# Kernel tuning notes

Hardware: AMD Instinct MI355X
Metric: run time of the kernel (lower is better)

Reference implementation:

```python
import jax, jax.numpy as jnp
import numpy as np
from jax import lax

B, C, H, W = 256, 64, 48, 48   # batch, in_channels, spatial_dim, spatial_dim
E = 5                           # num_experts (ConditionalConv2D default)
DIM = 64 + 1                    # n_regulators + 1


def setup_inputs() -> dict:
    key = jax.random.key(0)
    ks = jax.random.split(key, 24)
    def n(k, shape, s=0.05):
        return jax.random.normal(k, shape, jnp.float32) * s
    inp = {
        "spatial_maps": jax.random.normal(ks[0], (B, C, H, W), jnp.float32),
        "cluster_info": jax.random.randint(ks[1], (B,), 0, C),
        # ConditionalConv2D (1x1, num_experts=5)
        "expert_w": n(ks[2], (E, C, C)),          # [experts, out_c, in_c] (1x1 squeezed)
        "cond_b": n(ks[3], (C,)),
        "route_emb": n(ks[4], (C, 4 * C)),        # Embedding(num_clusters=C, pool_emb=4C)
        "route_W": n(ks[5], (E, 8 * C)),          # Linear(2*pool_emb -> E)
        "route_b": n(ks[6], (E,)),
        # weight-normed conv stack (v, g, bias, prelu-a)
        "v1": n(ks[7], (32, C, 3, 3)),  "g1": jnp.ones((32,), jnp.float32),  "cb1": n(ks[8], (32,)),  "a1": jnp.array(0.1, jnp.float32),
        "v2": n(ks[9], (64, 32, 3, 3)), "g2": jnp.ones((64,), jnp.float32),  "cb2": n(ks[10], (64,)), "a2": jnp.array(0.1, jnp.float32),
        "v3": n(ks[11], (128, 64, 3, 3)), "g3": jnp.ones((128,), jnp.float32), "cb3": n(ks[12], (128,)), "a3": jnp.array(0.1, jnp.float32),
        # cluster embedding + alpha + MLP
        "emb2": n(ks[13], (C, 128)),
        "alpha": jnp.array(1.0, jnp.float32),
        "mW1": n(ks[14], (64, 128)), "mb1": n(ks[15], (64,)), "a4": jnp.array(0.1, jnp.float32),
        "mW2": n(ks[16], (32, 64)),  "mb2": n(ks[17], (32,)), "a5": jnp.array(0.1, jnp.float32),
        "mW3": n(ks[18], (DIM, 32)), "mb3": n(ks[19], (DIM,)),
    }
    return inp


def _wn(v, g):
    # weight_norm over all dims except 0 (torch default dim=0)
    nrm = jnp.sqrt((v * v).sum((1, 2, 3)))
    return v * (g / nrm)[:, None, None, None]


def _conv(x, w, b):
    y = lax.conv_general_dilated(x, w, (1, 1), 'SAME',
                                 dimension_numbers=('NCHW', 'OIHW', 'NCHW'))
    return y + b[None, :, None, None]


def _prelu(x, a):
    return jnp.where(x >= 0, x, a * x)


def _mpool(x):
    return lax.reduce_window(x, -jnp.inf, lax.max, (1, 1, 2, 2), (1, 1, 2, 2), 'VALID')


def reference(spatial_maps, cluster_info, expert_w, cond_b, route_emb, route_W, route_b,
              v1, g1, cb1, a1, v2, g2, cb2, a2, v3, g3, cb3, a3,
              emb2, alpha, mW1, mb1, a4, mW2, mb2, a5, mW3, mb3):
    x = spatial_maps
    # routing: adaptive avg pool (2,2), flatten, concat cluster embedding, linear, sigmoid
    pooled = x.reshape(B, C, 2, H // 2, 2, W // 2).mean((3, 5)).reshape(B, 4 * C)
    feat = jnp.concatenate([pooled, route_emb[cluster_info]], axis=1)      # [B, 8C]
    rw = jax.nn.sigmoid(feat @ route_W.T + route_b)                        # [B, E]
    # per-sample expert-mixed 1x1 kernel, applied as batched 1x1 conv
    kern = jnp.einsum('be,eoi->boi', rw, expert_w)                         # [B, C, C]
    cc = jnp.einsum('boi,bihw->bohw', kern, x) + cond_b[None, :, None, None]
    out = jax.nn.sigmoid(cc) * x                                           # attention gate
    # dense conv stack
    h = _mpool(_prelu(_conv(out, _wn(v1, g1), cb1), a1))
    h = _mpool(_prelu(_conv(h, _wn(v2, g2), cb2), a2))
    h = _mpool(_prelu(_conv(h, _wn(v3, g3), cb3), a3))
    h = h.mean((2, 3))                                                      # AdaptiveAvgPool2d(1)+Flatten -> [B,128]
    h = h + emb2[cluster_info] * alpha
    # MLP head
    h = _prelu(h @ mW1.T + mb1, a4)
    h = _prelu(h @ mW2.T + mb2, a5)
    return h @ mW3.T + mb3                                                  # [B, DIM]
```

## Files before the change

### kernel.cpp

```cpp
#include <hip/hip_runtime.h>


typedef _Float16 f16;
typedef f16 f16x8 __attribute__((ext_vector_type(8)));
typedef f16 f16x4 __attribute__((ext_vector_type(4)));
typedef float f32x4 __attribute__((ext_vector_type(4)));

constexpr size_t OFF_POOLED = 0;
constexpr size_t OFF_KERN   = 65536;
constexpr size_t OFF_W1     = 65536 + 1048576;
constexpr size_t OFF_W2     = OFF_W1 + 32*64*12;
constexpr size_t OFF_W3     = OFF_W2 + 64*32*12;
constexpr size_t OFF_H1     = OFF_W3 + 128*64*12;

__device__ __forceinline__ float sigmoidf_(float z) {
    return 1.0f / (1.0f + __expf(-z));
}

__device__ __forceinline__ void store_slot8(f16* glds, int row, int sc, int icg, const float* c) {
    f16x8 hv = { (f16)c[0], (f16)c[1], (f16)c[2], (f16)c[3],
                 (f16)c[4], (f16)c[5], (f16)c[6], (f16)c[7] };
    *(f16x8*)&glds[(row * 50 + sc) * 64 + ((icg ^ (sc & 7)) << 3)] = hv;
}

__global__ void k_wnorm(const float* __restrict__ v1, const float* __restrict__ g1,
                        const float* __restrict__ v2, const float* __restrict__ g2,
                        const float* __restrict__ v3, const float* __restrict__ g3,
                        float* __restrict__ ws)
{
    int bo = blockIdx.x;
    const float* v; const float* g; int IC, oc; int which;
    if (bo < 32)       { v = v1; g = g1; oc = bo;      IC = 64; which = 1; }
    else if (bo < 96)  { v = v2; g = g2; oc = bo - 32; IC = 32; which = 2; }
    else               { v = v3; g = g3; oc = bo - 96; IC = 64; which = 3; }
    int n = IC * 9;
    const float* vo = v + (size_t)oc * n;
    float s = 0.0f;
    for (int i = threadIdx.x; i < n; i += 256) { float xv = vo[i]; s += xv * xv; }
    __shared__ float swarp[4];
    __shared__ float sscale;
    int lane = threadIdx.x & 63, wid = threadIdx.x >> 6;
    #pragma unroll
    for (int off = 32; off; off >>= 1) s += __shfl_down(s, off);
    if (lane == 0) swarp[wid] = s;
    __syncthreads();
    if (threadIdx.x == 0) {
        float tsum = swarp[0] + swarp[1] + swarp[2] + swarp[3];
        sscale = g[oc] / sqrtf(tsum);
    }
    __syncthreads();
    float sc = sscale;
    if (which == 1) {
        f16* o1 = (f16*)(ws + OFF_W1);
        for (int i = threadIdx.x; i < n; i += 256) {
            int ic = i / 9, kk = i - ic * 9;
            o1[kk * 2048 + oc * 64 + (ic ^ ((oc & 7) << 3))] = (f16)(vo[i] * sc);
        }
    } else if (which == 2) {
        f16* o2 = (f16*)(ws + OFF_W2);
        for (int i = threadIdx.x; i < n; i += 256) {
            int ic = i / 9, kk = i - ic * 9;
            o2[(kk * 64 + oc) * 32 + ic] = (f16)(vo[i] * sc);
        }
    } else {
        f16* o3 = (f16*)(ws + OFF_W3);
        for (int i = threadIdx.x; i < n; i += 256) {
            int ic = i / 9, kk = i - ic * 9;
            o3[(kk * 128 + oc) * 64 + ic] = (f16)(vo[i] * sc);
        }
    }
}

__global__ void __launch_bounds__(64)
k_pool(const float* __restrict__ x, float* __restrict__ ws)
{
    int bc = blockIdx.x;
    int lane = threadIdx.x;
    const float4* p = (const float4*)(x + (size_t)bc * 2304);
    float a0 = 0.f, a1 = 0.f, a2 = 0.f, a3 = 0.f;
    #pragma unroll
    for (int j = 0; j < 9; j++) {
        int i = lane + 64 * j;
        int row = i / 12, cg = i - 12 * row;
        float4 v = p[i];
        float s = v.x + v.y + v.z + v.w;
        bool hq = (row >= 24), wq = (cg >= 6);
        a0 += (!hq && !wq) ? s : 0.f;
        a1 += (!hq &&  wq) ? s : 0.f;
        a2 += ( hq && !wq) ? s : 0.f;
        a3 += ( hq &&  wq) ? s : 0.f;
    }
    #pragma unroll
    for (int off = 32; off; off >>= 1) {
        a0 += __shfl_down(a0, off);
        a1 += __shfl_down(a1, off);
        a2 += __shfl_down(a2, off);
        a3 += __shfl_down(a3, off);
    }
    if (lane == 0) {
        int b = bc >> 6, c = bc & 63;
        float* d = ws + OFF_POOLED + (size_t)b * 256 + c * 4;
        d[0] = a0 * (1.0f / 576.0f);
        d[1] = a1 * (1.0f / 576.0f);
        d[2] = a2 * (1.0f / 576.0f);
        d[3] = a3 * (1.0f / 576.0f);
    }
}

__global__ void k_route(const int* __restrict__ cluster,
                        const float* __restrict__ route_emb,
                        const float* __restrict__ route_W,
                        const float* __restrict__ route_b,
                        const float* __restrict__ expert_w,
                        float* __restrict__ ws)
{
    int b = blockIdx.x, t = threadIdx.x;
    __shared__ float feat[512];
    __shared__ float rwv[5];
    __shared__ float red[256];
    int cl = cluster[b];
    feat[t]       = ws[OFF_POOLED + (size_t)b * 256 + t];
    feat[256 + t] = route_emb[(size_t)cl * 256 + t];
    __syncthreads();
    float f0 = feat[t], f1 = feat[256 + t];
    for (int e = 0; e < 5; e++) {
        float pv = f0 * route_W[e * 512 + t] + f1 * route_W[e * 512 + 256 + t];
        red[t] = pv;
        __syncthreads();
        if (t < 128) red[t] += red[t + 128];
        __syncthreads();
        if (t < 64) {
            float s = red[t] + red[t + 64];
            #pragma unroll
            for (int off = 32; off; off >>= 1) s += __shfl_down(s, off);
            if (t == 0) rwv[e] = sigmoidf_(s + route_b[e]);
        }
        __syncthreads();
    }
    float r0 = rwv[0], r1 = rwv[1], r2 = rwv[2], r3 = rwv[3], r4 = rwv[4];
    f16* khg = (f16*)(ws + OFF_KERN);
    for (int j = t; j < 4096; j += 256) {
        int oc = j >> 6, ic = j & 63;
        float kv = r0 * expert_w[j] + r1 * expert_w[4096 + j] +
                   r2 * expert_w[2 * 4096 + j] + r3 * expert_w[3 * 4096 + j] +
                   r4 * expert_w[4 * 4096 + j];
        khg[(size_t)b * 4096 + oc * 64 + (ic ^ ((oc & 7) << 3))] = (f16)kv;
    }
}

__global__ void __launch_bounds__(512, 4)
k_f1(const float* __restrict__ x, const f16* __restrict__ kernH,
     const float* __restrict__ cond_b, const f16* __restrict__ w1H,
     const float* __restrict__ cb1, const float* __restrict__ a1,
     f16* __restrict__ h1h)
{
    extern __shared__ char smem[];
    f16*  glds  = (f16*)smem;
    f16*  kh    = (f16*)(smem + 64000);
    float* cbl  = (float*)(smem + 72192);
    float* dump = (float*)smem;
    f16*  poolt = (f16*)(smem + 52224);

    const int t = threadIdx.x;
    const int tile = blockIdx.x;
    const int b = blockIdx.y;
    const int r0 = tile * 8;
    const int w = t >> 6, l = t & 63;
    const int l15 = l & 15, agrp = l >> 4;

    ((uint4*)kh)[t] = ((const uint4*)(kernH + (size_t)b * 4096))[t];
    if (t < 64) cbl[t] = cond_b[t];
    if (t < 160) {
        int row = t >> 4, rem = t & 15;
        int col = (rem >= 8) ? 49 : 0;
        int slot = rem & 7;
        uint4 z = {};
        *(uint4*)&glds[(row * 50 + col) * 64 + slot * 8] = z;
    }
    for (int e = t; e < 960; e += 512) {
        int row = e / 96;
        int rem = e - row * 96;
        int colg = rem >> 3;
        int icg = rem & 7;
        int r_in = r0 - 1 + row;
        float4 va[8];
        if (r_in >= 0 && r_in < 48) {
            const float4* xp = (const float4*)x + ((size_t)(b * 64 + icg * 8)) * 576 + r_in * 12 + colg;
            #pragma unroll
            for (int i = 0; i < 8; i++) va[i] = xp[i * 576];
        } else {
            #pragma unroll
            for (int i = 0; i < 8; i++) va[i] = (float4){0.f, 0.f, 0.f, 0.f};
        }
        float c0[8], c1[8], c2c[8], c3[8];
        #pragma unroll
        for (int i = 0; i < 8; i++) { c0[i] = va[i].x; c1[i] = va[i].y; c2c[i] = va[i].z; c3[i] = va[i].w; }
        int scb = colg * 4 + 1;
        store_slot8(glds, row, scb + 0, icg, c0);
        store_slot8(glds, row, scb + 1, icg, c1);
        store_slot8(glds, row, scb + 2, icg, c2c);
        store_slot8(glds, row, scb + 3, icg, c3);
    }
    __syncthreads();

    {
        const int nt0 = (w < 6) ? 4 * w : 24 + 3 * (w - 6);
        const int NT  = (w < 6) ? 4 : 3;
        f32x4 acc[4][4] = {};
        int srA[4], scA[4];
        #pragma unroll
        for (int j = 0; j < 4; j++) {
            int ntc = nt0 + ((j < NT) ? j : 0);
            int p = ntc * 16 + l15;
            srA[j] = p / 48; scA[j] = p - 48 * srA[j] + 1;
        }
        #pragma unroll
        for (int ks = 0; ks < 2; ks++) {
            f16x8 kfr[4];
            #pragma unroll
            for (int mt = 0; mt < 4; mt++) {
                int oc = mt * 16 + l15;
                kfr[mt] = *(const f16x8*)&kh[oc * 64 + (((ks * 4 + agrp) ^ (oc & 7)) << 3)];
            }
            #pragma unroll
            for (int j = 0; j < 4; j++) {
                f16x8 bfr = *(const f16x8*)&glds[(srA[j] * 50 + scA[j]) * 64 +
                                                 (((ks * 4 + agrp) ^ (scA[j] & 7)) << 3)];
                #pragma unroll
                for (int mt = 0; mt < 4; mt++)
                    acc[mt][j] = __builtin_amdgcn_mfma_f32_16x16x32_f16(kfr[mt], bfr, acc[mt][j], 0, 0, 0);
            }
        }
        #pragma unroll
        for (int j = 0; j < 4; j++) {
            if (j < NT) {
                int base = (srA[j] * 50 + scA[j]) * 64;
                int sw8 = (scA[j] & 7) << 3;
                #pragma unroll
                for (int mt = 0; mt < 4; mt++) {
                    #pragma unroll
                    for (int rr = 0; rr < 4; rr++) {
                        int oc = mt * 16 + 4 * agrp + rr;
                        int addr = base + (oc ^ sw8);
                        float xv = (float)glds[addr];
                        float gg = sigmoidf_(acc[mt][j][rr] + cbl[oc]);
                        glds[addr] = (f16)(gg * xv);
                    }
                }
            }
        }
    }
    __syncthreads();

    f32x4 c2[3][2] = {};
    {
        const int q = w;
        #pragma unroll
        for (int kt = 0; kt < 18; kt++) {
            const int kk = kt >> 1, hh = kt & 1;
            const int dy = kk / 3, dx = kk - dy * 3;
            f16x8 bfr2[2];
            #pragma unroll
            for (int nt = 0; nt < 2; nt++) {
                int oc = nt * 16 + l15;
                int slot = (hh * 4 + agrp) ^ (oc & 7);
                bfr2[nt] = *(const f16x8*)&w1H[(kk * 32 + oc) * 64 + slot * 8];
            }
            #pragma unroll
            for (int mtl = 0; mtl < 3; mtl++) {
                int sc = mtl * 16 + l15 + dx;
                int slot = (hh * 4 + agrp) ^ (sc & 7);
                f16x8 af = *(const f16x8*)&glds[((q + dy) * 50 + sc) * 64 + slot * 8];
                c2[mtl][0] = __builtin_amdgcn_mfma_f32_16x16x32_f16(af, bfr2[0], c2[mtl][0], 0, 0, 0);
                c2[mtl][1] = __builtin_amdgcn_mfma_f32_16x16x32_f16(af, bfr2[1], c2[mtl][1], 0, 0, 0);
            }
        }
    }
    __syncthreads();

    {
        const int q = w;
        #pragma unroll
        for (int mtl = 0; mtl < 3; mtl++)
            #pragma unroll
            for (int nt = 0; nt < 2; nt++)
                #pragma unroll
                for (int rr = 0; rr < 4; rr++) {
                    int pcl = mtl * 16 + 4 * agrp + rr;
                    dump[(q * 48 + pcl) * 34 + nt * 16 + l15] = c2[mtl][nt][rr];
                }
    }
    __syncthreads();

    {
        const float av = a1[0];
        #pragma unroll
        for (int k = 0; k < 6; k++) {
            int e = t + 512 * k;
            int oc = e & 31, pos2 = e >> 5;
            int pr = pos2 / 24, pc = pos2 - 24 * pr;
            int p0 = (2 * pr) * 48 + 2 * pc;
            float m = fmaxf(fmaxf(dump[p0 * 34 + oc], dump[(p0 + 1) * 34 + oc]),
                            fmaxf(dump[(p0 + 48) * 34 + oc], dump[(p0 + 49) * 34 + oc]));
            float v = m + cb1[oc];
            v = (v >= 0.0f) ? v : av * v;
            poolt[pos2 * 40 + oc] = (f16)v;
        }
    }
    __syncthreads();

    if (t < 384) {
        int pos2 = t >> 2, slot = t & 3;
        uint4 val = *(const uint4*)&poolt[pos2 * 40 + slot * 8];
        ((uint4*)h1h)[((size_t)b * 576 + tile * 96 + pos2) * 4 + slot] = val;
    }
}

__global__ void __launch_bounds__(512, 1)
k_f23(const f16* __restrict__ h1h, const f16* __restrict__ w2h,
      const float* __restrict__ cb2, const float* __restrict__ a2,
      const f16* __restrict__ w3h, const float* __restrict__ cb3, const float* __restrict__ a3,
      const int* __restrict__ cluster, const float* __restrict__ emb2, const float* __restrict__ alpha,
      const float* __restrict__ mW1, const float* __restrict__ mb1, const float* __restrict__ a4,
      const float* __restrict__ mW2, const float* __restrict__ mb2, const float* __restrict__ a5,
      const float* __restrict__ mW3, const float* __restrict__ mb3,
      float* __restrict__ out)
{
    extern __shared__ char smem[];
    f16*  x2    = (f16*)smem;
    f16*  h2l   = (f16*)(smem + 82944);
    float* ps   = (float*)(smem + 111168);
    float* hb   = (float*)(smem + 113216);
    float* t1   = (float*)(smem + 113728);
    float* t2   = (float*)(smem + 113984);
    f16*  dump2 = (f16*)smem;
    f16*  dump3 = (f16*)smem;

    const int b = blockIdx.x, t = threadIdx.x;
    const int w = t >> 6, l = t & 63;
    const int l15 = l & 15, agrp = l >> 4;

    for (int e = t; e < 400; e += 512) {
        int bp = e >> 2, slot = e & 3;
        int r, c;
        if (bp < 26)      { r = 0;  c = bp; }
        else if (bp < 52) { r = 25; c = bp - 26; }
        else if (bp < 76) { r = bp - 52 + 1; c = 0; }
        else              { r = bp - 76 + 1; c = 25; }
        uint4 z = {};
        *(uint4*)&x2[(r * 26 + c) * 40 + slot * 8] = z;
    }
    for (int e = t; e < 416; e += 512) {
        int bp = e >> 3, slot = e & 7;
        int r, c;
        if (bp < 14)      { r = 0;  c = bp; }
        else if (bp < 28) { r = 13; c = bp - 14; }
        else if (bp < 40) { r = bp - 28 + 1; c = 0; }
        else              { r = bp - 40 + 1; c = 13; }
        uint4 z = {};
        *(uint4*)&h2l[(r * 14 + c) * 72 + slot * 8] = z;
    }
    {
        const uint4* src = (const uint4*)(h1h + (size_t)b * 18432);
        for (int e = t; e < 2304; e += 512) {
            int pos = e >> 2, slot = e & 3;
            int r = pos / 24, c = pos - 24 * r;
            *(uint4*)&x2[((r + 1) * 26 + (c + 1)) * 40 + slot * 8] = src[e];
        }
    }
    __syncthreads();

    const int m = w & 3, half = w >> 2;
    f32x4 acc[18];
    {
        f16x8 afr[9];
        #pragma unroll
        for (int kk = 0; kk < 9; kk++)
            afr[kk] = *(const f16x8*)&w2h[(kk * 64 + m * 16 + l15) * 32 + agrp * 8];
        #pragma unroll
        for (int nt = 0; nt < 18; nt++) acc[nt] = (f32x4){0.f, 0.f, 0.f, 0.f};
        constexpr int K2[9] = {0, 40, 80, 26 * 40, 27 * 40, 28 * 40, 52 * 40, 53 * 40, 54 * 40};
        #pragma unroll
        for (int nt = 0; nt < 18; nt++) {
            int p = (half * 18 + nt) * 16 + l15;
            int r = p / 24, c = p - 24 * r;
            int base = (r * 26 + c) * 40 + agrp * 8;
            #pragma unroll
            for (int kk = 0; kk < 9; kk++) {
                f16x8 bfr = *(const f16x8*)&x2[base + K2[kk]];
                acc[nt] = __builtin_amdgcn_mfma_f32_16x16x32_f16(afr[kk], bfr, acc[nt], 0, 0, 0);
            }
        }
    }
    __syncthreads();

    #pragma unroll
    for (int nt = 0; nt < 18; nt++) {
        int p = (half * 18 + nt) * 16 + l15;
        f16x4 hv = { (f16)acc[nt][0], (f16)acc[nt][1], (f16)acc[nt][2], (f16)acc[nt][3] };
        *(f16x4*)&dump2[p * 72 + m * 16 + 4 * agrp] = hv;
    }
    __syncthreads();

    {
        const float a2v = a2[0];
        for (int e = t; e < 9216; e += 512) {
            int oc = e & 63, pos2 = e >> 6;
            int pr = pos2 / 12, pc = pos2 - 12 * pr;
            int p0 = (2 * pr) * 24 + 2 * pc;
            float mm = fmaxf(fmaxf((float)dump2[p0 * 72 + oc], (float)dump2[(p0 + 1) * 72 + oc]),
                             fmaxf((float)dump2[(p0 + 24) * 72 + oc], (float)dump2[(p0 + 25) * 72 + oc]));
            float v = mm + cb2[oc];
            v = (v >= 0.0f) ? v : a2v * v;
            h2l[((pr + 1) * 14 + (pc + 1)) * 72 + oc] = (f16)v;
        }
    }
    __syncthreads();

    f32x4 acc9[9];
    {
        int pb[9];
        #pragma unroll
        for (int nt = 0; nt < 9; nt++) {
            int p = nt * 16 + l15;
            int r = p / 12, c = p - 12 * r;
            pb[nt] = (r * 14 + c) * 72 + agrp * 8;
            acc9[nt] = (f32x4){0.f, 0.f, 0.f, 0.f};
        }
        constexpr int K3[9] = {0, 72, 144, 14 * 72, 15 * 72, 16 * 72, 28 * 72, 29 * 72, 30 * 72};
        #pragma unroll
        for (int kk = 0; kk < 9; kk++) {
            #pragma unroll
            for (int ks = 0; ks < 2; ks++) {
                f16x8 afr = *(const f16x8*)&w3h[(size_t)(kk * 128 + w * 16 + l15) * 64 + ks * 32 + agrp * 8];
                #pragma unroll
                for (int nt = 0; nt < 9; nt++) {
                    f16x8 bfr = *(const f16x8*)&h2l[pb[nt] + ks * 32 + K3[kk]];
                    acc9[nt] = __builtin_amdgcn_mfma_f32_16x16x32_f16(afr, bfr, acc9[nt], 0, 0, 0);
                }
            }
        }
    }
    #pragma unroll
    for (int nt = 0; nt < 9; nt++) {
        int p = nt * 16 + l15;
        f16x4 hv = { (f16)acc9[nt][0], (f16)acc9[nt][1], (f16)acc9[nt][2], (f16)acc9[nt][3] };
        *(f16x4*)&dump3[p * 136 + w * 16 + 4 * agrp] = hv;
    }
    __syncthreads();

    {
        int oc = t >> 2, q = t & 3;
        int qr = q >> 1, qc = q & 1;
        const float a3v = a3[0];
        float cbv = cb3[oc];
        float s = 0.f;
        #pragma unroll
        for (int i = 0; i < 3; i++)
            #pragma unroll
            for (int j = 0; j < 3; j++) {
                int pr = 3 * qr + i, pc = 3 * qc + j;
                int p0 = (2 * pr) * 12 + 2 * pc;
                float mm = fmaxf(fmaxf((float)dump3[p0 * 136 + oc], (float)dump3[(p0 + 1) * 136 + oc]),
                                 fmaxf((float)dump3[(p0 + 12) * 136 + oc], (float)dump3[(p0 + 13) * 136 + oc]));
                float v = mm + cbv;
                v = (v >= 0.0f) ? v : a3v * v;
                s += v;
            }
        ps[t] = s;
    }
    __syncthreads();
    if (t < 128) {
        int cl = cluster[b];
        hb[t] = (ps[4 * t] + ps[4 * t + 1] + ps[4 * t + 2] + ps[4 * t + 3]) * (1.0f / 36.0f)
              + emb2[(size_t)cl * 128 + t] * alpha[0];
    }
    __syncthreads();
    if (t < 64) {
        const float4* wr = (const float4*)(mW1 + t * 128);
        float s = mb1[t];
        #pragma unroll 8
        for (int j = 0; j < 32; j++) {
            float4 wv4 = wr[j];
            s += wv4.x * hb[4 * j] + wv4.y * hb[4 * j + 1] + wv4.z * hb[4 * j + 2] + wv4.w * hb[4 * j + 3];
        }
        float a4v = a4[0];
        t1[t] = (s >= 0.0f) ? s : a4v * s;
    }
    __syncthreads();
    if (t < 32) {
        const float4* wr = (const float4*)(mW2 + t * 64);
        float s = mb2[t];
        #pragma unroll
        for (int j = 0; j < 16; j++) {
            float4 wv4 = wr[j];
            s += wv4.x * t1[4 * j] + wv4.y * t1[4 * j + 1] + wv4.z * t1[4 * j + 2] + wv4.w * t1[4 * j + 3];
        }
        float a5v = a5[0];
        t2[t] = (s >= 0.0f) ? s : a5v * s;
    }
    __syncthreads();
    if (t < 65) {
        const float4* wr = (const float4*)(mW3 + t * 32);
        float s = mb3[t];
        #pragma unroll
        for (int j = 0; j < 8; j++) {
            float4 wv4 = wr[j];
            s += wv4.x * t2[4 * j] + wv4.y * t2[4 * j + 1] + wv4.z * t2[4 * j + 2] + wv4.w * t2[4 * j + 3];
        }
        out[(size_t)b * 65 + t] = s;
    }
}

extern "C" void kernel_launch(void* const* d_in, const int* in_sizes, int n_in,
                              void* d_out, int out_size, void* d_ws, size_t ws_size,
                              hipStream_t stream)
{
    const float* x         = (const float*)d_in[0];
    const int*   cluster   = (const int*)  d_in[1];
    const float* expert_w  = (const float*)d_in[2];
    const float* cond_b    = (const float*)d_in[3];
    const float* route_emb = (const float*)d_in[4];
    const float* route_W   = (const float*)d_in[5];
    const float* route_b   = (const float*)d_in[6];
    const float* v1  = (const float*)d_in[7];
    const float* g1  = (const float*)d_in[8];
    const float* cb1 = (const float*)d_in[9];
    const float* a1  = (const float*)d_in[10];
    const float* v2  = (const float*)d_in[11];
    const float* g2  = (const float*)d_in[12];
    const float* cb2 = (const float*)d_in[13];
    const float* a2  = (const float*)d_in[14];
    const float* v3  = (const float*)d_in[15];
    const float* g3  = (const float*)d_in[16];
    const float* cb3 = (const float*)d_in[17];
    const float* a3  = (const float*)d_in[18];
    const float* emb2  = (const float*)d_in[19];
    const float* alpha = (const float*)d_in[20];
    const float* mW1 = (const float*)d_in[21];
    const float* mb1 = (const float*)d_in[22];
    const float* a4  = (const float*)d_in[23];
    const float* mW2 = (const float*)d_in[24];
    const float* mb2 = (const float*)d_in[25];
    const float* a5  = (const float*)d_in[26];
    const float* mW3 = (const float*)d_in[27];
    const float* mb3 = (const float*)d_in[28];
    float* ws  = (float*)d_ws;
    float* out = (float*)d_out;

    hipFuncSetAttribute((const void*)k_f1,  hipFuncAttributeMaxDynamicSharedMemorySize, 72448);
    hipFuncSetAttribute((const void*)k_f23, hipFuncAttributeMaxDynamicSharedMemorySize, 114112);

    k_wnorm<<<224, 256, 0, stream>>>(v1, g1, v2, g2, v3, g3, ws);
    k_pool<<<16384, 64, 0, stream>>>(x, ws);
    k_route<<<256, 256, 0, stream>>>(cluster, route_emb, route_W, route_b, expert_w, ws);
    k_f1<<<dim3(6, 256), 512, 72448, stream>>>(x, (const f16*)(ws + OFF_KERN), cond_b,
                                               (const f16*)(ws + OFF_W1), cb1, a1,
                                               (f16*)(ws + OFF_H1));
    k_f23<<<256, 512, 114112, stream>>>((const f16*)(ws + OFF_H1), (const f16*)(ws + OFF_W2),
                                        cb2, a2, (const f16*)(ws + OFF_W3), cb3, a3,
                                        cluster, emb2, alpha,
                                        mW1, mb1, a4, mW2, mb2, a5, mW3, mb3, out);
}
```

Before: 131.4 us.

## Pre-reduce horizontal maxpool in registers, pack fp16 conversions, vectorize gating

```diff
diff --git a/kernel.cpp b/kernel.cpp
--- a/kernel.cpp
+++ b/kernel.cpp
@@ -4,6 +4,8 @@
 typedef _Float16 f16;
 typedef f16 f16x8 __attribute__((ext_vector_type(8)));
 typedef f16 f16x4 __attribute__((ext_vector_type(4)));
+typedef f16 f16x2 __attribute__((ext_vector_type(2)));
+typedef __fp16 h16x2 __attribute__((ext_vector_type(2)));
 typedef float f32x4 __attribute__((ext_vector_type(4)));
 
 constexpr size_t OFF_POOLED = 0;
@@ -14,12 +16,21 @@
 constexpr size_t OFF_H1     = OFF_W3 + 128*64*12;
 
 __device__ __forceinline__ float sigmoidf_(float z) {
-    return 1.0f / (1.0f + __expf(-z));
+    return __builtin_amdgcn_rcpf(1.0f + __expf(-z));
+}
+
+__device__ __forceinline__ f16x2 pkrtz(float a, float b) {
+    h16x2 r = __builtin_amdgcn_cvt_pkrtz(a, b);
+    f16x2 o; o[0] = (f16)r[0]; o[1] = (f16)r[1];
+    return o;
 }
 
 __device__ __forceinline__ void store_slot8(f16* glds, int row, int sc, int icg, const float* c) {
-    f16x8 hv = { (f16)c[0], (f16)c[1], (f16)c[2], (f16)c[3],
-                 (f16)c[4], (f16)c[5], (f16)c[6], (f16)c[7] };
+    f16x2 p0 = pkrtz(c[0], c[1]);
+    f16x2 p1 = pkrtz(c[2], c[3]);
+    f16x2 p2 = pkrtz(c[4], c[5]);
+    f16x2 p3 = pkrtz(c[6], c[7]);
+    f16x8 hv = { p0[0], p0[1], p1[0], p1[1], p2[0], p2[1], p3[0], p3[1] };
     *(f16x8*)&glds[(row * 50 + sc) * 64 + ((icg ^ (sc & 7)) << 3)] = hv;
 }
 
@@ -133,7 +144,7 @@
             float s = red[t] + red[t + 64];
             #pragma unroll
             for (int off = 32; off; off >>= 1) s += __shfl_down(s, off);
-            if (t == 0) rwv[e] = sigmoidf_(s + route_b[e]);
+            if (t == 0) rwv[e] = 1.0f / (1.0f + __expf(-(s + route_b[e])));
         }
         __syncthreads();
     }
@@ -158,8 +169,8 @@
     f16*  glds  = (f16*)smem;
     f16*  kh    = (f16*)(smem + 64000);
     float* cbl  = (float*)(smem + 72192);
-    float* dump = (float*)smem;
-    f16*  poolt = (f16*)(smem + 52224);
+    f16*  hm    = (f16*)smem;
+    f16*  poolt = (f16*)(smem + 16384);
 
     const int t = threadIdx.x;
     const int tile = blockIdx.x;
@@ -231,6 +242,9 @@
                     acc[mt][j] = __builtin_amdgcn_mfma_f32_16x16x32_f16(kfr[mt], bfr, acc[mt][j], 0, 0, 0);
             }
         }
+        f32x4 cbv[4];
+        #pragma unroll
+        for (int mt = 0; mt < 4; mt++) cbv[mt] = *(const f32x4*)&cbl[mt * 16 + 4 * agrp];
         #pragma unroll
         for (int j = 0; j < 4; j++) {
             if (j < NT) {
@@ -238,14 +252,21 @@
                 int sw8 = (scA[j] & 7) << 3;
                 #pragma unroll
                 for (int mt = 0; mt < 4; mt++) {
-                    #pragma unroll
-                    for (int rr = 0; rr < 4; rr++) {
-                        int oc = mt * 16 + 4 * agrp + rr;
-                        int addr = base + (oc ^ sw8);
-                        float xv = (float)glds[addr];
-                        float gg = sigmoidf_(acc[mt][j][rr] + cbl[oc]);
-                        glds[addr] = (f16)(gg * xv);
-                    }
+                    int oc0 = mt * 16 + 4 * agrp;
+                    int addr = base + (oc0 ^ sw8);
+                    f16x4 xv4 = *(const f16x4*)&glds[addr];
+                    float s0 = sigmoidf_(acc[mt][j][0] + cbv[mt][0]);
+                    float s1 = sigmoidf_(acc[mt][j][1] + cbv[mt][1]);
+                    float s2 = sigmoidf_(acc[mt][j][2] + cbv[mt][2]);
+                    float s3 = sigmoidf_(acc[mt][j][3] + cbv[mt][3]);
+                    f16x2 slo = pkrtz(s0, s1);
+                    f16x2 shi = pkrtz(s2, s3);
+                    f16x2 xlo = { xv4[0], xv4[1] };
+                    f16x2 xhi = { xv4[2], xv4[3] };
+                    f16x2 glo = slo * xlo;
+                    f16x2 ghi = shi * xhi;
+                    f16x4 g4 = { glo[0], glo[1], ghi[0], ghi[1] };
+                    *(f16x4*)&glds[addr] = g4;
                 }
             }
         }
@@ -283,12 +304,14 @@
         #pragma unroll
         for (int mtl = 0; mtl < 3; mtl++)
             #pragma unroll
-            for (int nt = 0; nt < 2; nt++)
-                #pragma unroll
-                for (int rr = 0; rr < 4; rr++) {
-                    int pcl = mtl * 16 + 4 * agrp + rr;
-                    dump[(q * 48 + pcl) * 34 + nt * 16 + l15] = c2[mtl][nt][rr];
-                }
+            for (int nt = 0; nt < 2; nt++) {
+                float h0 = fmaxf(c2[mtl][nt][0], c2[mtl][nt][1]);
+                float h1 = fmaxf(c2[mtl][nt][2], c2[mtl][nt][3]);
+                f16x2 hp = pkrtz(h0, h1);
+                int oc = nt * 16 + l15;
+                int pp = mtl * 8 + 2 * agrp;
+                *(f16x2*)&hm[(q * 32 + oc) * 26 + pp] = hp;
+            }
     }
     __syncthreads();
 
@@ -299,10 +322,9 @@
             int e = t + 512 * k;
             int oc = e & 31, pos2 = e >> 5;
             int pr = pos2 / 24, pc = pos2 - 24 * pr;
-            int p0 = (2 * pr) * 48 + 2 * pc;
-            float m = fmaxf(fmaxf(dump[p0 * 34 + oc], dump[(p0 + 1) * 34 + oc]),
-                            fmaxf(dump[(p0 + 48) * 34 + oc], dump[(p0 + 49) * 34 + oc]));
-            float v = m + cb1[oc];
+            float v0 = (float)hm[((2 * pr) * 32 + oc) * 26 + pc];
+            float v1 = (float)hm[((2 * pr + 1) * 32 + oc) * 26 + pc];
+            float v = fmaxf(v0, v1) + cb1[oc];
             v = (v >= 0.0f) ? v : av * v;
             poolt[pos2 * 40 + oc] = (f16)v;
         }
@@ -397,7 +419,9 @@
     #pragma unroll
     for (int nt = 0; nt < 18; nt++) {
         int p = (half * 18 + nt) * 16 + l15;
-        f16x4 hv = { (f16)acc[nt][0], (f16)acc[nt][1], (f16)acc[nt][2], (f16)acc[nt][3] };
+        f16x2 d0 = pkrtz(acc[nt][0], acc[nt][1]);
+        f16x2 d1 = pkrtz(acc[nt][2], acc[nt][3]);
+        f16x4 hv = { d0[0], d0[1], d1[0], d1[1] };
         *(f16x4*)&dump2[p * 72 + m * 16 + 4 * agrp] = hv;
     }
     __syncthreads();
@@ -444,7 +468,9 @@
     #pragma unroll
     for (int nt = 0; nt < 9; nt++) {
         int p = nt * 16 + l15;
-        f16x4 hv = { (f16)acc9[nt][0], (f16)acc9[nt][1], (f16)acc9[nt][2], (f16)acc9[nt][3] };
+        f16x2 d0 = pkrtz(acc9[nt][0], acc9[nt][1]);
+        f16x2 d1 = pkrtz(acc9[nt][2], acc9[nt][3]);
+        f16x4 hv = { d0[0], d0[1], d1[0], d1[1] };
         *(f16x4*)&dump3[p * 136 + w * 16 + 4 * agrp] = hv;
     }
     __syncthreads();
```

Result: faster. 121.1 us (-7.8%).
